# Kernel optimization log

Hardware: AMD Instinct MI355X
Metric: run time of the kernel (lower is better)

The kernel has to match this reference:

```python
import jax, jax.numpy as jnp
import numpy as np

B, T, D_Q, D_K, D_W = 128, 4096, 16, 16, 32


def setup_inputs() -> dict:
    key0 = jax.random.key(0)
    ks = jax.random.split(key0, 8)
    return {
        "query": jax.random.normal(ks[0], (B, 1, D_Q), dtype=jnp.float32),
        "key": jax.random.normal(ks[1], (B, T, D_K), dtype=jnp.float32),
        "value": jax.random.normal(ks[2], (B, T, D_K), dtype=jnp.float32),
        "W1": jax.random.normal(ks[3], (D_W, D_Q), dtype=jnp.float32) * 0.1,
        "W2": jax.random.normal(ks[4], (D_W, D_K), dtype=jnp.float32) * 0.1,
        "bias": jax.random.uniform(ks[5], (), dtype=jnp.float32, minval=-0.1, maxval=0.1),
        "v_w": jax.random.normal(ks[6], (1, D_W), dtype=jnp.float32) * 0.1,
        "v_b": jax.random.normal(ks[7], (1,), dtype=jnp.float32) * 0.1,
    }


def reference(query, key, value, W1, W2, bias, v_w, v_b):
    # Bahdanau additive attention.
    # query: [B,1,d_q], key/value: [B,T,d_k]
    q_proj = jnp.einsum('bqd,wd->bqw', query, W1)      # [B,1,d_w]
    k_proj = jnp.einsum('btd,wd->btw', key, W2)        # [B,T,d_w]
    h = jnp.tanh(k_proj + q_proj + bias)               # [B,T,d_w]
    score = (jnp.einsum('btw,ow->bto', h, v_w) + v_b).squeeze(-1)  # [B,T]
    attn = jax.nn.softmax(score, axis=-1)              # [B,T]
    context = jnp.einsum('bt,btd->bd', attn, value)[:, None, :]    # [B,1,d_v]
    return context, attn
```

## Files before the change

kernel.cpp:

```cpp
#include <hip/hip_runtime.h>

#define NB 128
#define NT 4096
#define DKD 16
#define DW 32
#define CHUNKS 8
#define TC 512
#define BLK 256
#define PT 2
#define BLK2 128

__device__ __forceinline__ float fast_tanh(float x) {
    float e = __expf(2.0f * x);
    return 1.0f - 2.0f * __builtin_amdgcn_rcpf(e + 1.0f);
}

__global__ __launch_bounds__(BLK, 4) void aa_score(
    const float* __restrict__ query, const float* __restrict__ key,
    const float* __restrict__ value, const float* __restrict__ W1,
    const float* __restrict__ W2, const float* __restrict__ bias,
    const float* __restrict__ v_w, const float* __restrict__ v_b,
    float* __restrict__ attn,
    float* __restrict__ ws_l,
    float* __restrict__ ws_ctx)
{
    const int b   = blockIdx.x >> 3;
    const int c   = blockIdx.x & 7;
    const int tid = threadIdx.x;

    __shared__ float s_comb[DW];
    __shared__ float s_rctx[4 * 16];
    __shared__ float s_rl[4];

    if (tid < DW) {
        const int w = tid;
        float acc = bias[0];
        const float* q  = query + b * DKD;
        const float* w1 = W1 + w * DKD;
        #pragma unroll
        for (int d = 0; d < DKD; ++d) acc = fmaf(q[d], w1[d], acc);
        s_comb[w] = acc;
    }

    const size_t tbase = (size_t)b * NT + (size_t)c * TC + (size_t)tid * PT;
    const float4* kp = reinterpret_cast<const float4*>(key)   + tbase * 4;
    const float4* vp = reinterpret_cast<const float4*>(value) + tbase * 4;

    float4 ka[PT][4], va[PT][4];
    #pragma unroll
    for (int j = 0; j < PT; ++j) {
        #pragma unroll
        for (int r = 0; r < 4; ++r) ka[j][r] = kp[4*j + r];
    }
    #pragma unroll
    for (int j = 0; j < PT; ++j) {
        #pragma unroll
        for (int r = 0; r < 4; ++r) va[j][r] = vp[4*j + r];
    }

    __syncthreads();

    const float vb = v_b[0];
    float sc[PT];
    #pragma unroll
    for (int j = 0; j < PT; ++j) sc[j] = vb;

    #pragma unroll
    for (int w = 0; w < DW; ++w) {
        const float* wr = W2 + w * DKD;
        const float cw  = s_comb[w];
        const float vww = v_w[w];
        #pragma unroll
        for (int j = 0; j < PT; ++j) {
            float h = cw;
            h = fmaf(ka[j][0].x, wr[ 0], h); h = fmaf(ka[j][0].y, wr[ 1], h);
            h = fmaf(ka[j][0].z, wr[ 2], h); h = fmaf(ka[j][0].w, wr[ 3], h);
            h = fmaf(ka[j][1].x, wr[ 4], h); h = fmaf(ka[j][1].y, wr[ 5], h);
            h = fmaf(ka[j][1].z, wr[ 6], h); h = fmaf(ka[j][1].w, wr[ 7], h);
            h = fmaf(ka[j][2].x, wr[ 8], h); h = fmaf(ka[j][2].y, wr[ 9], h);
            h = fmaf(ka[j][2].z, wr[10], h); h = fmaf(ka[j][2].w, wr[11], h);
            h = fmaf(ka[j][3].x, wr[12], h); h = fmaf(ka[j][3].y, wr[13], h);
            h = fmaf(ka[j][3].z, wr[14], h); h = fmaf(ka[j][3].w, wr[15], h);
            sc[j] = fmaf(fast_tanh(h), vww, sc[j]);
        }
    }

    float l = 0.0f;
    float ctx[16];
    #pragma unroll
    for (int d = 0; d < 16; ++d) ctx[d] = 0.0f;

    float p[PT];
    #pragma unroll
    for (int j = 0; j < PT; ++j) {
        p[j] = __expf(sc[j]);
        l += p[j];
        #pragma unroll
        for (int r = 0; r < 4; ++r) {
            ctx[4*r+0] = fmaf(p[j], va[j][r].x, ctx[4*r+0]);
            ctx[4*r+1] = fmaf(p[j], va[j][r].y, ctx[4*r+1]);
            ctx[4*r+2] = fmaf(p[j], va[j][r].z, ctx[4*r+2]);
            ctx[4*r+3] = fmaf(p[j], va[j][r].w, ctx[4*r+3]);
        }
    }
    reinterpret_cast<float2*>(attn + (size_t)b * NT + (size_t)c * TC)[tid] =
        make_float2(p[0], p[1]);

    #pragma unroll
    for (int o = 32; o > 0; o >>= 1) l += __shfl_xor(l, o);
    #pragma unroll
    for (int d = 0; d < 16; ++d) {
        #pragma unroll
        for (int o = 32; o > 0; o >>= 1) ctx[d] += __shfl_xor(ctx[d], o);
    }
    const int wave = tid >> 6;
    const int lane = tid & 63;
    if (lane == 0) {
        s_rl[wave] = l;
        #pragma unroll
        for (int d = 0; d < 16; ++d) s_rctx[wave * 16 + d] = ctx[d];
    }
    __syncthreads();
    const int slot = b * CHUNKS + c;
    if (tid < 16)
        ws_ctx[slot * 16 + tid] =
            s_rctx[tid] + s_rctx[16 + tid] + s_rctx[32 + tid] + s_rctx[48 + tid];
    if (tid == 0)
        ws_l[slot] = s_rl[0] + s_rl[1] + s_rl[2] + s_rl[3];
}

__global__ __launch_bounds__(BLK2) void aa_finish(
    float* __restrict__ out,
    const float* __restrict__ ws_l,
    const float* __restrict__ ws_ctx)
{
    const int b   = blockIdx.x >> 3;
    const int c   = blockIdx.x & 7;
    const int tid = threadIdx.x;
    float L = 0.0f;
    #pragma unroll
    for (int i = 0; i < CHUNKS; ++i) L += ws_l[b * CHUNKS + i];
    const float inv = 1.0f / L;

    float4* ap = reinterpret_cast<float4*>(out + NB*DKD + (size_t)b * NT + (size_t)c * TC);
    float4 p = ap[tid];
    p.x *= inv; p.y *= inv; p.z *= inv; p.w *= inv;
    ap[tid] = p;

    if (c == 0 && tid < DKD) {
        const float* wc = ws_ctx + b * CHUNKS * 16;
        float s = 0.0f;
        #pragma unroll
        for (int i = 0; i < CHUNKS; ++i) s += wc[i * 16 + tid];
        out[b * DKD + tid] = s * inv;
    }
}

extern "C" void kernel_launch(void* const* d_in, const int* in_sizes, int n_in,
                              void* d_out, int out_size, void* d_ws, size_t ws_size,
                              hipStream_t stream) {
    const float* query = (const float*)d_in[0];
    const float* key   = (const float*)d_in[1];
    const float* value = (const float*)d_in[2];
    const float* W1    = (const float*)d_in[3];
    const float* W2    = (const float*)d_in[4];
    const float* bias  = (const float*)d_in[5];
    const float* v_w   = (const float*)d_in[6];
    const float* v_b   = (const float*)d_in[7];
    float* out = (float*)d_out;

    float* ws_l   = (float*)d_ws;
    float* ws_ctx = ws_l + NB * CHUNKS;

    aa_score<<<NB * CHUNKS, BLK, 0, stream>>>(
        query, key, value, W1, W2, bias, v_w, v_b,
        out + NB * DKD, ws_l, ws_ctx);
    aa_finish<<<NB * CHUNKS, BLK2, 0, stream>>>(out, ws_l, ws_ctx);
}
```

Measured before the change: 119.3 us.

## Process one timestep per thread with more chunks and defer value loads

Halves the work per thread (one timestep instead of two) and doubles the number of chunks per batch, so 2048 blocks are launched, and raises the launch-bounds occupancy hint from 4 to 6. Value loads now happen after the score computation, and key loads are issued before the query projection, which shrinks the live register set. The aim is more waves in flight to hide memory latency. In exchange there is twice the cross-wave reduction and shuffle overhead per timestep, and the value-load latency is exposed later in the kernel.

```diff
diff --git a/kernel.cpp b/kernel.cpp
--- a/kernel.cpp
+++ b/kernel.cpp
@@ -4,10 +4,9 @@
 #define NT 4096
 #define DKD 16
 #define DW 32
-#define CHUNKS 8
-#define TC 512
+#define CHUNKS 16
+#define TC 256
 #define BLK 256
-#define PT 2
 #define BLK2 128
 
 __device__ __forceinline__ float fast_tanh(float x) {
@@ -15,7 +14,7 @@
     return 1.0f - 2.0f * __builtin_amdgcn_rcpf(e + 1.0f);
 }
 
-__global__ __launch_bounds__(BLK, 4) void aa_score(
+__global__ __launch_bounds__(BLK, 6) void aa_score(
     const float* __restrict__ query, const float* __restrict__ key,
     const float* __restrict__ value, const float* __restrict__ W1,
     const float* __restrict__ W2, const float* __restrict__ bias,
@@ -24,13 +23,18 @@
     float* __restrict__ ws_l,
     float* __restrict__ ws_ctx)
 {
-    const int b   = blockIdx.x >> 3;
-    const int c   = blockIdx.x & 7;
+    const int b   = blockIdx.x >> 4;
+    const int c   = blockIdx.x & 15;
     const int tid = threadIdx.x;
 
     __shared__ float s_comb[DW];
     __shared__ float s_rctx[4 * 16];
     __shared__ float s_rl[4];
+
+    const size_t tbase = (size_t)b * NT + (size_t)c * TC + tid;
+    const float4* kp = reinterpret_cast<const float4*>(key)   + tbase * 4;
+    const float4* vp = reinterpret_cast<const float4*>(value) + tbase * 4;
+    const float4 k0 = kp[0], k1 = kp[1], k2 = kp[2], k3 = kp[3];
 
     if (tid < DW) {
         const int w = tid;
@@ -41,71 +45,37 @@
         for (int d = 0; d < DKD; ++d) acc = fmaf(q[d], w1[d], acc);
         s_comb[w] = acc;
     }
-
-    const size_t tbase = (size_t)b * NT + (size_t)c * TC + (size_t)tid * PT;
-    const float4* kp = reinterpret_cast<const float4*>(key)   + tbase * 4;
-    const float4* vp = reinterpret_cast<const float4*>(value) + tbase * 4;
-
-    float4 ka[PT][4], va[PT][4];
-    #pragma unroll
-    for (int j = 0; j < PT; ++j) {
-        #pragma unroll
-        for (int r = 0; r < 4; ++r) ka[j][r] = kp[4*j + r];
-    }
-    #pragma unroll
-    for (int j = 0; j < PT; ++j) {
-        #pragma unroll
-        for (int r = 0; r < 4; ++r) va[j][r] = vp[4*j + r];
-    }
-
     __syncthreads();
 
     const float vb = v_b[0];
-    float sc[PT];
-    #pragma unroll
-    for (int j = 0; j < PT; ++j) sc[j] = vb;
+    float sc = vb;
 
     #pragma unroll
     for (int w = 0; w < DW; ++w) {
         const float* wr = W2 + w * DKD;
-        const float cw  = s_comb[w];
-        const float vww = v_w[w];
-        #pragma unroll
-        for (int j = 0; j < PT; ++j) {
-            float h = cw;
-            h = fmaf(ka[j][0].x, wr[ 0], h); h = fmaf(ka[j][0].y, wr[ 1], h);
-            h = fmaf(ka[j][0].z, wr[ 2], h); h = fmaf(ka[j][0].w, wr[ 3], h);
-            h = fmaf(ka[j][1].x, wr[ 4], h); h = fmaf(ka[j][1].y, wr[ 5], h);
-            h = fmaf(ka[j][1].z, wr[ 6], h); h = fmaf(ka[j][1].w, wr[ 7], h);
-            h = fmaf(ka[j][2].x, wr[ 8], h); h = fmaf(ka[j][2].y, wr[ 9], h);
-            h = fmaf(ka[j][2].z, wr[10], h); h = fmaf(ka[j][2].w, wr[11], h);
-            h = fmaf(ka[j][3].x, wr[12], h); h = fmaf(ka[j][3].y, wr[13], h);
-            h = fmaf(ka[j][3].z, wr[14], h); h = fmaf(ka[j][3].w, wr[15], h);
-            sc[j] = fmaf(fast_tanh(h), vww, sc[j]);
-        }
+        float h = s_comb[w];
+        h = fmaf(k0.x, wr[ 0], h); h = fmaf(k0.y, wr[ 1], h);
+        h = fmaf(k0.z, wr[ 2], h); h = fmaf(k0.w, wr[ 3], h);
+        h = fmaf(k1.x, wr[ 4], h); h = fmaf(k1.y, wr[ 5], h);
+        h = fmaf(k1.z, wr[ 6], h); h = fmaf(k1.w, wr[ 7], h);
+        h = fmaf(k2.x, wr[ 8], h); h = fmaf(k2.y, wr[ 9], h);
+        h = fmaf(k2.z, wr[10], h); h = fmaf(k2.w, wr[11], h);
+        h = fmaf(k3.x, wr[12], h); h = fmaf(k3.y, wr[13], h);
+        h = fmaf(k3.z, wr[14], h); h = fmaf(k3.w, wr[15], h);
+        sc = fmaf(fast_tanh(h), v_w[w], sc);
     }
 
-    float l = 0.0f;
+    const float p = __expf(sc);
+    attn[(size_t)b * NT + (size_t)c * TC + tid] = p;
+
+    const float4 v0 = vp[0], v1 = vp[1], v2 = vp[2], v3 = vp[3];
     float ctx[16];
-    #pragma unroll
-    for (int d = 0; d < 16; ++d) ctx[d] = 0.0f;
+    ctx[ 0] = p * v0.x; ctx[ 1] = p * v0.y; ctx[ 2] = p * v0.z; ctx[ 3] = p * v0.w;
+    ctx[ 4] = p * v1.x; ctx[ 5] = p * v1.y; ctx[ 6] = p * v1.z; ctx[ 7] = p * v1.w;
+    ctx[ 8] = p * v2.x; ctx[ 9] = p * v2.y; ctx[10] = p * v2.z; ctx[11] = p * v2.w;
+    ctx[12] = p * v3.x; ctx[13] = p * v3.y; ctx[14] = p * v3.z; ctx[15] = p * v3.w;
 
-    float p[PT];
-    #pragma unroll
-    for (int j = 0; j < PT; ++j) {
-        p[j] = __expf(sc[j]);
-        l += p[j];
-        #pragma unroll
-        for (int r = 0; r < 4; ++r) {
-            ctx[4*r+0] = fmaf(p[j], va[j][r].x, ctx[4*r+0]);
-            ctx[4*r+1] = fmaf(p[j], va[j][r].y, ctx[4*r+1]);
-            ctx[4*r+2] = fmaf(p[j], va[j][r].z, ctx[4*r+2]);
-            ctx[4*r+3] = fmaf(p[j], va[j][r].w, ctx[4*r+3]);
-        }
-    }
-    reinterpret_cast<float2*>(attn + (size_t)b * NT + (size_t)c * TC)[tid] =
-        make_float2(p[0], p[1]);
-
+    float l = p;
     #pragma unroll
     for (int o = 32; o > 0; o >>= 1) l += __shfl_xor(l, o);
     #pragma unroll
@@ -135,19 +105,19 @@
     const float* __restrict__ ws_ctx)
 {
     const int b   = blockIdx.x >> 3;
-    const int c   = blockIdx.x & 7;
+    const int seg = blockIdx.x & 7;
     const int tid = threadIdx.x;
     float L = 0.0f;
     #pragma unroll
     for (int i = 0; i < CHUNKS; ++i) L += ws_l[b * CHUNKS + i];
     const float inv = 1.0f / L;
 
-    float4* ap = reinterpret_cast<float4*>(out + NB*DKD + (size_t)b * NT + (size_t)c * TC);
+    float4* ap = reinterpret_cast<float4*>(out + NB*DKD + (size_t)b * NT + (size_t)seg * 512);
     float4 p = ap[tid];
     p.x *= inv; p.y *= inv; p.z *= inv; p.w *= inv;
     ap[tid] = p;
 
-    if (c == 0 && tid < DKD) {
+    if (seg == 0 && tid < DKD) {
         const float* wc = ws_ctx + b * CHUNKS * 16;
         float s = 0.0f;
         #pragma unroll
@@ -175,5 +145,5 @@
     aa_score<<<NB * CHUNKS, BLK, 0, stream>>>(
         query, key, value, W1, W2, bias, v_w, v_b,
         out + NB * DKD, ws_l, ws_ctx);
-    aa_finish<<<NB * CHUNKS, BLK2, 0, stream>>>(out, ws_l, ws_ctx);
+    aa_finish<<<NB * 8, BLK2, 0, stream>>>(out, ws_l, ws_ctx);
 }
```

Measured after the change: 120.1 us. Within noise of the previous version (+0.7%).
